# Kernel optimization log

Hardware: AMD Instinct MI355X
Metric: run time of the kernel (lower is better)

Reference implementation:

```python
import jax, jax.numpy as jnp
import numpy as np

B, T, V = 128, 257, 1024   # T = U + 1 (structural constraint of the module)
U = 256
N_EMB, D_EMB = 1000, 512
NEG = -1e30
BLANK = 0


def setup_inputs() -> dict:
    key = jax.random.key(0)
    k0, k1, k2, k3, k4 = jax.random.split(key, 5)
    x = jax.random.normal(k0, (B, T, V), jnp.float32)
    y = jax.random.randint(k1, (B, U), 1, N_EMB, dtype=jnp.int32)  # labels in [1, 999], never blank
    xlen = jnp.full((B,), T, jnp.int32)
    ylen = jnp.full((B,), U, jnp.int32)
    embed_w = jax.random.normal(k2, (N_EMB, D_EMB), jnp.float32)
    lin_w = jax.random.normal(k3, (V, D_EMB), jnp.float32) / np.float32(np.sqrt(D_EMB))
    lin_b = jax.random.normal(k4, (V,), jnp.float32) * 0.01
    return {"x": x, "xlen": xlen, "y": y, "ylen": ylen,
            "embed_w": embed_w, "lin_w": lin_w, "lin_b": lin_b}


def _ctc_loss_sum(lp, targets, xlen, ylen):
    # lp: [T, B, V] treated as log-probs (faithful to the original, which feeds raw
    # logits straight into torch.nn.CTCLoss). targets: [B, U] padded with blank.
    Tn, Bn, _ = lp.shape
    Un = targets.shape[1]
    S = 2 * Un + 1
    # extended label sequence: blank, y1, blank, y2, ..., blank   -> [B, S]
    ext = jnp.full((Bn, S), BLANK, targets.dtype).at[:, 1::2].set(targets)
    bidx = jnp.arange(Bn)[:, None]
    lp_ext = lp[:, bidx, ext]                       # [T, B, S]
    # skip transition s-2 -> s allowed iff ext[s] != blank and ext[s] != ext[s-2]
    ext_m2 = jnp.pad(ext, ((0, 0), (2, 0)), constant_values=-1)[:, :S]
    skip_ok = (ext != BLANK) & (ext != ext_m2)      # [B, S]

    def lse3(a, b, c):
        m = jnp.maximum(jnp.maximum(a, b), c)
        return m + jnp.log(jnp.exp(a - m) + jnp.exp(b - m) + jnp.exp(c - m))

    alpha0 = (jnp.full((Bn, S), NEG, lp.dtype)
              .at[:, 0].set(lp_ext[0, :, 0])
              .at[:, 1].set(lp_ext[0, :, 1]))

    def step(alpha, lp_t):
        a1 = jnp.pad(alpha, ((0, 0), (1, 0)), constant_values=NEG)[:, :S]
        a2 = jnp.pad(alpha, ((0, 0), (2, 0)), constant_values=NEG)[:, :S]
        a2 = jnp.where(skip_ok, a2, NEG)
        new = lp_t + lse3(alpha, a1, a2)
        return new, new

    _, rest = jax.lax.scan(step, alpha0, lp_ext[1:])
    alphas = jnp.concatenate([alpha0[None], rest], axis=0)   # [T, B, S]
    aT = alphas[xlen - 1, jnp.arange(Bn)]                    # [B, S] at each seq's last frame
    s_last = 2 * ylen                                        # final blank position
    ll = jnp.logaddexp(aT[jnp.arange(Bn), s_last],
                       aT[jnp.arange(Bn), s_last - 1])
    return -jnp.sum(ll)                                      # reduction='sum'


def reference(x, xlen, y, ylen, embed_w, lin_w, lin_b):
    # mask padded label positions to blank (make_pad_mask + masked_fill_)
    pad = jnp.arange(y.shape[1], dtype=ylen.dtype)[None, :] >= ylen[:, None]
    y = jnp.where(pad, 0, y)
    z = jnp.concatenate([jnp.zeros((y.shape[0], 1), y.dtype), y], axis=1)  # [B, U+1]
    h = embed_w[z]                                   # [B, T, 512]
    logits = x + h @ lin_w.T + lin_b                 # [B, T, 1024]
    log_probs = jnp.transpose(logits, (1, 0, 2))     # [T, B, V]
    return _ctc_loss_sum(log_probs, y, xlen, ylen)
```

## Files before the change

kernel.cpp:

```cpp
#include <hip/hip_runtime.h>

#define NEG (-1e30f)

constexpr int B_ = 128;
constexpr int T_ = 257;
constexpr int V_ = 1024;
constexpr int U_ = 256;
constexpr int DE_ = 512;
constexpr int NWAVE_ = B_ * T_;


__global__ __launch_bounds__(256) void gather_kernel(const float* __restrict__ x,
                                                     const int* __restrict__ y,
                                                     const int* __restrict__ ylen,
                                                     const float* __restrict__ E,
                                                     const float* __restrict__ L,
                                                     const float* __restrict__ bias,
                                                     float4* __restrict__ V)
{
    const int wave = (blockIdx.x << 2) | (threadIdx.x >> 6);
    if (wave >= NWAVE_) return;
    const int lane = threadIdx.x & 63;
    const int t = wave >> 7;
    const int b = wave & 127;

    const int yl = ylen[b];
    int ym1 = 0, yt = 0, ym2 = 0;
    if (t >= 1 && (t - 1) < yl) ym1 = y[b * U_ + t - 1];
    if (t <= 255 && t < yl)     yt  = y[b * U_ + t];
    if (t >= 2 && (t - 2) < yl) ym2 = y[b * U_ + t - 2];
    const int z = (t == 0) ? 0 : ym1;

    const float* xrow = x + ((size_t)b * T_ + t) * V_;
    const float xb0 = xrow[0];
    const float xbz = xrow[z];
    const float xbh = xrow[yt];

    const float4* Ez = (const float4*)(E + (size_t)z * DE_);
    const float4* L0 = (const float4*)L;
    const float4* Lz = (const float4*)(L + (size_t)z * DE_);
    const float4* Lh = (const float4*)(L + (size_t)yt * DE_);
    float s_bl = 0.f, s_lo = 0.f, s_hi = 0.f;
    #pragma unroll
    for (int h = 0; h < 2; ++h) {
        const int idx = lane + h * 64;
        const float4 e = Ez[idx];
        const float4 l0 = L0[idx], lz = Lz[idx], lh = Lh[idx];
        s_bl += e.x * l0.x + e.y * l0.y + e.z * l0.z + e.w * l0.w;
        s_lo += e.x * lz.x + e.y * lz.y + e.z * lz.z + e.w * lz.w;
        s_hi += e.x * lh.x + e.y * lh.y + e.z * lh.z + e.w * lh.w;
    }
    #pragma unroll
    for (int m = 1; m < 64; m <<= 1) {
        s_bl += __shfl_xor(s_bl, m, 64);
        s_lo += __shfl_xor(s_lo, m, 64);
        s_hi += __shfl_xor(s_hi, m, 64);
    }

    if (lane == 0) {
        const float v_bl = xb0 + s_bl + bias[0];
        const float v_lo = (t >= 1) ? (xbz + s_lo + bias[z]) : NEG;
        const float v_hi = xbh + s_hi + bias[yt];
        int flags = 0;
        if (t >= 1 && t <= 255 && yt != 0 && yt != ym1) flags |= 1;
        if (t >= 2 && ym1 != 0 && ym1 != ym2)           flags |= 2;
        const int g = b >> 4, j = b & 15;
        V[((size_t)(g * 257 + t) << 4) + j] =
            make_float4(v_lo, v_bl, v_hi, __int_as_float(flags));
    }
}

__global__ __launch_bounds__(256) void ctc_scan_kernel(const float4* __restrict__ V,
                                                       float* __restrict__ out)
{
    __shared__ __align__(16) float4 buf[256][16];
    const int tid = threadIdx.x;
    const int g = blockIdx.x;
    const float4* Vg = V + (size_t)g * 257 * 16;

    #pragma unroll
    for (int k = 0; k < 16; ++k) {
        const int idx = tid + k * 256;
        ((float4*)buf)[idx] = Vg[16 + idx];
    }
    __syncthreads();

    if (tid < 16) {
        const float4 f0 = Vg[tid];
        float lo = NEG, mid = f0.y, hi = f0.z;
        #pragma unroll 8
        for (int t = 1; t <= 256; ++t) {
            const float4 f = buf[t - 1][tid];
            const int flags = __float_as_int(f.w);
            const float nh = f.z + ((flags & 1) ? hi : NEG);
            const float nm = f.y + hi;
            const float a2 = (flags & 2) ? lo : NEG;
            const float m = fmaxf(fmaxf(hi, mid), a2);
            const float nl = f.x + m +
                __logf(__expf(hi - m) + __expf(mid - m) + __expf(a2 - m));
            hi = nh; mid = nm; lo = nl;
        }
        const float mm = fmaxf(mid, lo);
        float ll = mm + __logf(__expf(mid - mm) + __expf(lo - mm));
        #pragma unroll
        for (int m = 1; m < 16; m <<= 1) ll += __shfl_xor(ll, m, 64);
        if (tid == 0) atomicAdd(out, -ll);
    }
}

extern "C" void kernel_launch(void* const* d_in, const int* in_sizes, int n_in,
                              void* d_out, int out_size, void* d_ws, size_t ws_size,
                              hipStream_t stream)
{
    const float* x       = (const float*)d_in[0];
    const int*   y       = (const int*)  d_in[2];
    const int*   ylen    = (const int*)  d_in[3];
    const float* embed_w = (const float*)d_in[4];
    const float* lin_w   = (const float*)d_in[5];
    const float* lin_b   = (const float*)d_in[6];

    float4* V  = (float4*)d_ws;
    float* out = (float*)d_out;

    hipMemsetAsync(out, 0, sizeof(float), stream);
    const int nblk = (NWAVE_ + 3) / 4;
    gather_kernel<<<dim3(nblk), dim3(256), 0, stream>>>(
        x, y, ylen, embed_w, lin_w, lin_b, V);
    ctc_scan_kernel<<<dim3(8), dim3(256), 0, stream>>>(V, out);
}
```

Baseline: 224.1 us.

## Precompute per-token blank and diagonal logit tables in a separate kernel

```diff
diff --git a/kernel.cpp b/kernel.cpp
--- a/kernel.cpp
+++ b/kernel.cpp
@@ -6,9 +6,44 @@
 constexpr int T_ = 257;
 constexpr int V_ = 1024;
 constexpr int U_ = 256;
+constexpr int NE_ = 1000;
 constexpr int DE_ = 512;
 constexpr int NWAVE_ = B_ * T_;
 
+
+__global__ __launch_bounds__(256) void table_kernel(const float* __restrict__ E,
+                                                    const float* __restrict__ L,
+                                                    const float* __restrict__ bias,
+                                                    float* __restrict__ D0,
+                                                    float* __restrict__ Dd,
+                                                    float* __restrict__ out)
+{
+    if (blockIdx.x == 0 && threadIdx.x == 0) out[0] = 0.f;
+    const int m = (blockIdx.x << 2) | (threadIdx.x >> 6);
+    if (m >= NE_) return;
+    const int lane = threadIdx.x & 63;
+    const float4* Em = (const float4*)(E + (size_t)m * DE_);
+    const float4* L0 = (const float4*)L;
+    const float4* Lm = (const float4*)(L + (size_t)m * DE_);
+    float s0 = 0.f, sd = 0.f;
+    #pragma unroll
+    for (int h = 0; h < 2; ++h) {
+        const int idx = lane + h * 64;
+        const float4 e = Em[idx];
+        const float4 l0 = L0[idx], lm = Lm[idx];
+        s0 += e.x * l0.x + e.y * l0.y + e.z * l0.z + e.w * l0.w;
+        sd += e.x * lm.x + e.y * lm.y + e.z * lm.z + e.w * lm.w;
+    }
+    #pragma unroll
+    for (int msk = 1; msk < 64; msk <<= 1) {
+        s0 += __shfl_xor(s0, msk, 64);
+        sd += __shfl_xor(sd, msk, 64);
+    }
+    if (lane == 0) {
+        D0[m] = s0 + bias[0];
+        Dd[m] = sd + bias[m];
+    }
+}
 
 __global__ __launch_bounds__(256) void gather_kernel(const float* __restrict__ x,
                                                      const int* __restrict__ y,
@@ -16,6 +51,8 @@
                                                      const float* __restrict__ E,
                                                      const float* __restrict__ L,
                                                      const float* __restrict__ bias,
+                                                     const float* __restrict__ D0,
+                                                     const float* __restrict__ Dd,
                                                      float4* __restrict__ V)
 {
     const int wave = (blockIdx.x << 2) | (threadIdx.x >> 6);
@@ -35,32 +72,28 @@
     const float xb0 = xrow[0];
     const float xbz = xrow[z];
     const float xbh = xrow[yt];
+    const float d0z = D0[z];
+    const float ddz = Dd[z];
+    const float bh  = bias[yt];
 
     const float4* Ez = (const float4*)(E + (size_t)z * DE_);
-    const float4* L0 = (const float4*)L;
-    const float4* Lz = (const float4*)(L + (size_t)z * DE_);
     const float4* Lh = (const float4*)(L + (size_t)yt * DE_);
-    float s_bl = 0.f, s_lo = 0.f, s_hi = 0.f;
+    float s_hi = 0.f;
     #pragma unroll
     for (int h = 0; h < 2; ++h) {
         const int idx = lane + h * 64;
         const float4 e = Ez[idx];
-        const float4 l0 = L0[idx], lz = Lz[idx], lh = Lh[idx];
-        s_bl += e.x * l0.x + e.y * l0.y + e.z * l0.z + e.w * l0.w;
-        s_lo += e.x * lz.x + e.y * lz.y + e.z * lz.z + e.w * lz.w;
+        const float4 lh = Lh[idx];
         s_hi += e.x * lh.x + e.y * lh.y + e.z * lh.z + e.w * lh.w;
     }
     #pragma unroll
-    for (int m = 1; m < 64; m <<= 1) {
-        s_bl += __shfl_xor(s_bl, m, 64);
-        s_lo += __shfl_xor(s_lo, m, 64);
-        s_hi += __shfl_xor(s_hi, m, 64);
-    }
+    for (int msk = 1; msk < 64; msk <<= 1)
+        s_hi += __shfl_xor(s_hi, msk, 64);
 
     if (lane == 0) {
-        const float v_bl = xb0 + s_bl + bias[0];
-        const float v_lo = (t >= 1) ? (xbz + s_lo + bias[z]) : NEG;
-        const float v_hi = xbh + s_hi + bias[yt];
+        const float v_bl = xb0 + d0z;
+        const float v_lo = (t >= 1) ? (xbz + ddz) : NEG;
+        const float v_hi = xbh + s_hi + bh;
         int flags = 0;
         if (t >= 1 && t <= 255 && yt != 0 && yt != ym1) flags |= 1;
         if (t >= 2 && ym1 != 0 && ym1 != ym2)           flags |= 2;
@@ -120,11 +153,14 @@
     const float* lin_b   = (const float*)d_in[6];
 
     float4* V  = (float4*)d_ws;
-    float* out = (float*)d_out;
+    float*  D0 = (float*)((char*)d_ws + (size_t)8 * 257 * 16 * sizeof(float4));
+    float*  Dd = D0 + 1024;
+    float*  out = (float*)d_out;
 
-    hipMemsetAsync(out, 0, sizeof(float), stream);
+    table_kernel<<<dim3((NE_ + 3) / 4), dim3(256), 0, stream>>>(
+        embed_w, lin_w, lin_b, D0, Dd, out);
     const int nblk = (NWAVE_ + 3) / 4;
     gather_kernel<<<dim3(nblk), dim3(256), 0, stream>>>(
-        x, y, ylen, embed_w, lin_w, lin_b, V);
+        x, y, ylen, embed_w, lin_w, lin_b, D0, Dd, V);
     ctc_scan_kernel<<<dim3(8), dim3(256), 0, stream>>>(V, out);
 }
```

Result: no change. 220.3 us (-1.7%).
